# Kernel tuning notes

Measured on AMD Instinct MI355X. Metric: run time of the kernel, lower is better.

## Reference

```python
import jax, jax.numpy as jnp
import numpy as np

EPS = 1e-3  # keras BatchNormalization epsilon=0.001
CLIP = 20.0

def bn(x, g, b, m, v):
    # inference-mode batch norm over last axis
    return (x - m) * jax.lax.rsqrt(v + EPS) * g + b

def conv1d_relu(x, w, b, stride):
    # x: [B,T,C], w: [K,Cin,Cout], VALID padding, relu
    y = jax.lax.conv_general_dilated(x, w, (stride,), 'VALID',
                                     dimension_numbers=('NWC', 'WIO', 'NWC'))
    return jax.nn.relu(y + b)

def gru_dir(xp, Wh, bh, reverse):
    # xp: [B,T,3H] precomputed input projection (x@Wx + input bias)
    # keras GRU, reset_after=True, activation=relu, recurrent_activation=sigmoid
    B, T, H3 = xp.shape
    H = H3 // 3
    def step(h, xt):
        mh = h @ Wh + bh                       # [B,3H]
        xz, xr, xh = jnp.split(xt, 3, axis=-1)
        rz, rr, rh = jnp.split(mh, 3, axis=-1)
        z = jax.nn.sigmoid(xz + rz)
        r = jax.nn.sigmoid(xr + rr)
        hh = jax.nn.relu(xh + r * rh)
        h = z * h + (1.0 - z) * hh
        return h, h
    xs = jnp.swapaxes(xp, 0, 1)                # [T,B,3H]
    h0 = jnp.zeros((B, H), xp.dtype)
    _, ys = jax.lax.scan(step, h0, xs, reverse=reverse)
    return jnp.swapaxes(ys, 0, 1)              # [B,T,H]

def bi_gru_sum(x, Wx, Wh, b):
    # Wx: [2,in,3H], Wh: [2,H,3H], b: [2,2,3H] (input bias, recurrent bias)
    out = None
    for d in range(2):
        xp = x @ Wx[d] + b[d, 0]
        y = gru_dir(xp, Wh[d], b[d, 1], reverse=(d == 1))
        out = y if out is None else out + y
    return out


def setup_inputs() -> dict:
    key = jax.random.key(0)
    ks = jax.random.split(key, 16)
    B, T, F = 16, 1600, 80
    C = 512      # conv filters / gru units / fc units
    K = 5        # kernel size
    L = 3        # bi_gru layers
    V = 6000     # output_dim
    def rn(k, shape, s):
        return (jax.random.normal(k, shape, jnp.float32) * s)
    inp = {
        'x': rn(ks[0], (B, T, F), 1.0),
        'bn1_g': jnp.ones((F,), jnp.float32), 'bn1_b': jnp.zeros((F,), jnp.float32),
        'bn1_m': rn(ks[1], (F,), 0.1), 'bn1_v': jnp.ones((F,), jnp.float32),
        'conv_w0': rn(ks[2], (K, F, C), 0.05), 'conv_b0': jnp.zeros((C,), jnp.float32),
        'conv_w1': rn(ks[3], (K, C, C), 0.02), 'conv_b1': jnp.zeros((C,), jnp.float32),
        'bn2_g': jnp.ones((C,), jnp.float32), 'bn2_b': jnp.zeros((C,), jnp.float32),
        'bn2_m': rn(ks[4], (C,), 0.1), 'bn2_v': jnp.ones((C,), jnp.float32),
        # stacked GRU params: [layers, 2 dirs, ...]; relu recurrence -> small init
        'gru_wx': rn(ks[5], (L, 2, C, 3 * C), 0.03),
        'gru_wh': rn(ks[6], (L, 2, C, 3 * C), 0.03),
        'gru_b': jnp.zeros((L, 2, 2, 3 * C), jnp.float32),
        'bn3_g': jnp.ones((C,), jnp.float32), 'bn3_b': jnp.zeros((C,), jnp.float32),
        'bn3_m': rn(ks[7], (C,), 0.1), 'bn3_v': jnp.ones((C,), jnp.float32),
        'fc_w': rn(ks[8], (C, C), 0.04), 'fc_b': jnp.zeros((C,), jnp.float32),
        'sm_w': rn(ks[9], (C, V), 0.04), 'sm_b': jnp.zeros((V,), jnp.float32),
    }
    return inp


def reference(x, bn1_g, bn1_b, bn1_m, bn1_v,
              conv_w0, conv_b0, conv_w1, conv_b1,
              bn2_g, bn2_b, bn2_m, bn2_v,
              gru_wx, gru_wh, gru_b,
              bn3_g, bn3_b, bn3_m, bn3_v,
              fc_w, fc_b, sm_w, sm_b):
    x = bn(x, bn1_g, bn1_b, bn1_m, bn1_v)
    x = conv1d_relu(x, conv_w0, conv_b0, 2)    # [B,798,512]
    x = conv1d_relu(x, conv_w1, conv_b1, 2)    # [B,397,512]
    x = bn(x, bn2_g, bn2_b, bn2_m, bn2_v)
    for l in range(gru_wx.shape[0]):
        x = bi_gru_sum(x, gru_wx[l], gru_wh[l], gru_b[l])
    x = bn(x, bn3_g, bn3_b, bn3_m, bn3_v)
    x = jnp.minimum(jax.nn.relu(x @ fc_w + fc_b), CLIP)  # clipped_relu(max=20)
    return jax.nn.softmax(x @ sm_w + sm_b, axis=-1)      # [B,397,6000]
```

## Files before the change

kernel.cpp:

```cpp
#include <hip/hip_runtime.h>
#include <math.h>

using bf16x8 = __attribute__((ext_vector_type(8))) short;
using f32x4  = __attribute__((ext_vector_type(4))) float;
typedef unsigned short u16;
typedef unsigned int   u32;

#define EPSBN 1e-3f

__device__ __forceinline__ u16 f2bf(float f){
  union { float f; u32 u; } c; c.f = f;
  u32 u = c.u + 0x7fffu + ((c.u >> 16) & 1u);
  return (u16)(u >> 16);
}
__device__ __forceinline__ float bf2f(u16 b){
  union { u32 u; float f; } c; c.u = ((u32)b) << 16; return c.f;
}
__device__ __forceinline__ void splitstore(float v, u16* ph, u16* pl){
  u16 h = f2bf(v); *ph = h; *pl = f2bf(v - bf2f(h));
}
__device__ __forceinline__ f32x4 MFMA(bf16x8 a, bf16x8 b, f32x4 c){
  return __builtin_amdgcn_mfma_f32_16x16x32_bf16(a, b, c, 0, 0, 0);
}

__device__ __forceinline__ bf16x8 ld128_sys(const u16* p){
  bf16x8 r;
  asm volatile("global_load_dwordx4 %0, %1, off sc0 sc1" : "=v"(r) : "v"(p) : "memory");
  return r;
}
__device__ __forceinline__ void st16_sys(u16* p, u16 v){
  u32 vv = v;
  asm volatile("global_store_short %0, %1, off sc0 sc1" :: "v"(p), "v"(vv) : "memory");
}

__global__ __launch_bounds__(256) void k_bn1_split(
    const float* __restrict__ x, const float* __restrict__ g, const float* __restrict__ b,
    const float* __restrict__ m, const float* __restrict__ v,
    u16* __restrict__ oh, u16* __restrict__ ol)
{
  int i = blockIdx.x*256 + threadIdx.x;
  if (i >= 2048000) return;
  int ci = i % 80;
  float s = g[ci] * rsqrtf(v[ci] + EPSBN);
  float val = (x[i] - m[ci]) * s + b[ci];
  splitstore(val, oh+i, ol+i);
}

__global__ __launch_bounds__(256) void k_prep_c1w(
    const float* __restrict__ w0, u16* __restrict__ oh, u16* __restrict__ ol)
{
  int i = blockIdx.x*256 + threadIdx.x;
  if (i >= 512*416) return;
  int co = i / 416, kf = i - co*416;
  float val = 0.f;
  if (kf < 400){ int kw = kf/80, ci = kf - kw*80; val = w0[(kw*80+ci)*512 + co]; }
  splitstore(val, oh+i, ol+i);
}

__global__ __launch_bounds__(256) void k_prep_c2w(
    const float* __restrict__ w1, u16* __restrict__ oh, u16* __restrict__ ol)
{
  int i = blockIdx.x*256 + threadIdx.x;
  if (i >= 5*512*512) return;
  int co = i & 511, ci = (i >> 9) & 511, kw = i >> 18;
  long o = (long)co*2560 + kw*512 + ci;
  splitstore(w1[i], oh+o, ol+o);
}

__global__ __launch_bounds__(256) void k_prep_wx(
    const float* __restrict__ wx, const float* __restrict__ g2, const float* __restrict__ v2,
    u16* __restrict__ oh, u16* __restrict__ ol)
{
  long i = (long)blockIdx.x*256 + threadIdx.x;
  if (i >= 6L*512*1536) return;
  int n = (int)(i % 1536); long r2 = i / 1536; int k = (int)(r2 % 512); int ld = (int)(r2 / 512);
  float s = (ld < 2) ? g2[k]*rsqrtf(v2[k]+EPSBN) : 1.f;
  long o = ((long)ld*1536 + n)*512 + k;
  splitstore(wx[i]*s, oh+o, ol+o);
}

__global__ __launch_bounds__(256) void k_prep_wh(
    const float* __restrict__ wh, u16* __restrict__ oh, u16* __restrict__ ol)
{
  long i = (long)blockIdx.x*256 + threadIdx.x;
  if (i >= 6L*512*1536) return;
  int n = (int)(i % 1536); long r2 = i / 1536; int k = (int)(r2 % 512); int ld = (int)(r2 / 512);
  long o = ((long)ld*1536 + n)*512 + k;
  splitstore(wh[i], oh+o, ol+o);
}

__global__ __launch_bounds__(256) void k_prep_grub(
    const float* __restrict__ gb, const float* __restrict__ wx,
    const float* __restrict__ g2, const float* __restrict__ b2,
    const float* __restrict__ m2, const float* __restrict__ v2,
    float* __restrict__ xbias, float* __restrict__ hbias)
{
  int i = blockIdx.x*256 + threadIdx.x;
  if (i >= 6*1536) return;
  int n = i % 1536, ld = i / 1536;
  float xv = gb[(ld*2 + 0)*1536 + n];
  float hv = gb[(ld*2 + 1)*1536 + n];
  if (ld < 2){
    float acc = 0.f;
    for (int k = 0; k < 512; ++k){
      float s = g2[k]*rsqrtf(v2[k]+EPSBN);
      float t = b2[k] - m2[k]*s;
      acc += t * wx[((long)ld*512 + k)*1536 + n];
    }
    xv += acc;
  }
  xbias[i] = xv; hbias[i] = hv;
}

__global__ __launch_bounds__(256) void k_prep_fcw(
    const float* __restrict__ fw, const float* __restrict__ g3, const float* __restrict__ v3,
    u16* __restrict__ oh, u16* __restrict__ ol)
{
  int i = blockIdx.x*256 + threadIdx.x;
  if (i >= 512*512) return;
  int n = i & 511, k = i >> 9;
  float s = g3[k]*rsqrtf(v3[k]+EPSBN);
  long o = (long)n*512 + k;
  splitstore(fw[i]*s, oh+o, ol+o);
}

__global__ __launch_bounds__(256) void k_prep_fcb(
    const float* __restrict__ fw, const float* __restrict__ fb,
    const float* __restrict__ g3, const float* __restrict__ b3,
    const float* __restrict__ m3, const float* __restrict__ v3,
    float* __restrict__ ob)
{
  int n = blockIdx.x*256 + threadIdx.x;
  if (n >= 512) return;
  float acc = fb[n];
  for (int k = 0; k < 512; ++k){
    float s = g3[k]*rsqrtf(v3[k]+EPSBN);
    float t = b3[k] - m3[k]*s;
    acc += t * fw[k*512 + n];
  }
  ob[n] = acc;
}

__global__ __launch_bounds__(256) void k_prep_smw(
    const float* __restrict__ sw, u16* __restrict__ oh, u16* __restrict__ ol)
{
  long i = (long)blockIdx.x*256 + threadIdx.x;
  if (i >= 512L*6000) return;
  int n = (int)(i % 6000); int k = (int)(i / 6000);
  long o = (long)n*512 + k;
  splitstore(sw[i], oh+o, ol+o);
}

__global__ __launch_bounds__(256) void k_sumsplit(
    const float* __restrict__ a, const float* __restrict__ b,
    u16* __restrict__ oh, u16* __restrict__ ol)
{
  int i = blockIdx.x*256 + threadIdx.x;
  if (i >= 6352*512) return;
  splitstore(a[i] + b[i], oh+i, ol+i);
}

template<int AMODE, int EPI>
__global__ __launch_bounds__(256,1)
void gemm_split(const u16* __restrict__ Ah, const u16* __restrict__ Al,
                const u16* __restrict__ Bh, const u16* __restrict__ Bl,
                const float* __restrict__ bias,
                float* __restrict__ outF, u16* __restrict__ outH, u16* __restrict__ outL,
                int M, int N, int K, int Kvalid, int TIN, int TOUT)
{
  constexpr int CW = (AMODE==1) ? 80 : 512;
  const int tid  = threadIdx.x;
  const int lane = tid & 63;
  const int w    = tid >> 6;
  const int wm = w >> 1, wn = w & 1;
  const int r  = lane & 15, kg = lane >> 4;
  const int m0 = blockIdx.y * 64 + wm * 32;
  const int n0 = blockIdx.x * 64 + wn * 32;

  long abase[2];
  #pragma unroll
  for (int mt = 0; mt < 2; ++mt){
    int m = m0 + mt*16 + r;
    int mc = m < M ? m : M - 1;
    if (AMODE == 0) abase[mt] = (long)mc * K;
    else { int bb = mc / TOUT; int tt = mc - bb * TOUT; abase[mt] = ((long)bb * TIN + 2*tt) * CW; }
  }
  long bbase[2];
  #pragma unroll
  for (int nt = 0; nt < 2; ++nt){
    int n = n0 + nt*16 + r;
    int nc = n < N ? n : N - 1;
    bbase[nt] = (long)nc * K;
  }

  f32x4 acc[2][2];
  #pragma unroll
  for (int a_ = 0; a_ < 2; ++a_)
    #pragma unroll
    for (int b_ = 0; b_ < 2; ++b_) acc[a_][b_] = f32x4{0.f,0.f,0.f,0.f};

  const bf16x8 zfrag = {0,0,0,0,0,0,0,0};
  const int koff = kg * 8;
  const int KT = K >> 5;
  for (int kt = 0; kt < KT; ++kt){
    int kf = kt*32 + koff;
    bf16x8 ah[2], al[2], bh[2], bl[2];
    #pragma unroll
    for (int nt = 0; nt < 2; ++nt){
      bh[nt] = *(const bf16x8*)(Bh + bbase[nt] + kf);
      bl[nt] = *(const bf16x8*)(Bl + bbase[nt] + kf);
    }
    #pragma unroll
    for (int mt = 0; mt < 2; ++mt){
      if (AMODE == 0){
        long ao = abase[mt] + kf;
        ah[mt] = *(const bf16x8*)(Ah + ao); al[mt] = *(const bf16x8*)(Al + ao);
      } else {
        if (kf < Kvalid){
          int kw = kf / CW; int ci = kf - kw*CW;
          long ao = abase[mt] + (long)kw*CW + ci;
          ah[mt] = *(const bf16x8*)(Ah + ao); al[mt] = *(const bf16x8*)(Al + ao);
        } else { ah[mt] = zfrag; al[mt] = zfrag; }
      }
    }
    #pragma unroll
    for (int mt = 0; mt < 2; ++mt)
      #pragma unroll
      for (int nt = 0; nt < 2; ++nt){
        acc[mt][nt] = MFMA(ah[mt], bh[nt], acc[mt][nt]);
        acc[mt][nt] = MFMA(ah[mt], bl[nt], acc[mt][nt]);
        acc[mt][nt] = MFMA(al[mt], bh[nt], acc[mt][nt]);
      }
  }

  #pragma unroll
  for (int nt = 0; nt < 2; ++nt){
    int n = n0 + nt*16 + r;
    if (n >= N) continue;
    float bv = bias ? bias[n] : 0.f;
    #pragma unroll
    for (int mt = 0; mt < 2; ++mt){
      #pragma unroll
      for (int q = 0; q < 4; ++q){
        int m = m0 + mt*16 + kg*4 + q;
        if (m >= M) continue;
        float v = acc[mt][nt][q] + bv;
        if (EPI == 1) v = fmaxf(v, 0.f);
        if (EPI == 2) v = fminf(fmaxf(v, 0.f), 20.f);
        long o = (long)m * N + n;
        if (EPI == 0) outF[o] = v;
        else { u16 h = f2bf(v); outH[o] = h; outL[o] = f2bf(v - bf2f(h)); }
      }
    }
  }
}

__global__ __launch_bounds__(256,1)
void gru_layer(const float* __restrict__ xp,
               const u16* __restrict__ WhH, const u16* __restrict__ WhL,
               const float* __restrict__ hbias,
               float* __restrict__ yf, float* __restrict__ yb,
               u16* __restrict__ hbH_, u16* __restrict__ hbL_,
               u32* __restrict__ flags)
{
  const int dir = blockIdx.x >> 5;
  const int s   = blockIdx.x & 31;
  const int tid = threadIdx.x, lane = tid & 63, w = tid >> 6;
  const int r = lane & 15, kg = lane >> 4;

  const float* xpd = xp + (long)dir * (6352L*1536);
  const u16* whh = WhH + (long)dir * (1536L*512);
  const u16* whl = WhL + (long)dir * (1536L*512);
  const float* hb = hbias + dir * 1536;
  float* y = dir ? yb : yf;
  u16* hbH = hbH_ + dir * (2*8192);
  u16* hbL = hbL_ + dir * (2*8192);
  u32* flg = flags + dir * 32;

  __shared__ float red[4][3][64][4];

  bf16x8 Bh[3][4], Bl[3][4];
  #pragma unroll
  for (int g = 0; g < 3; ++g){
    long nb = (long)(g*512 + s*16 + r) * 512;
    #pragma unroll
    for (int kk = 0; kk < 4; ++kk){
      int k = (w*4 + kk)*32 + kg*8;
      Bh[g][kk] = *(const bf16x8*)(whh + nb + k);
      Bl[g][kk] = *(const bf16x8*)(whl + nb + k);
    }
  }

  const int gb = tid >> 4, gj = tid & 15;
  const int gcol = s*16 + gj;
  const float bz = hb[gcol], br = hb[512 + gcol], bhh = hb[1024 + gcol];
  const int rl = ((gb >> 2) << 4) | gj;
  const int rq = gb & 3;
  const int rb = r * 512 + kg * 8;
  float hreg = 0.f;

  for (int t = 0; t < 397; ++t){
    #pragma unroll
    for (int g = 0; g < 3; ++g)
      #pragma unroll
      for (int kk = 0; kk < 4; ++kk)
        asm volatile("" : "+v"(Bh[g][kk]), "+v"(Bl[g][kk]));

    const int tpos = dir ? (396 - t) : t;
    const long xb_ = ((long)gb*397 + tpos)*1536 + gcol;
    float xz = xpd[xb_], xr = xpd[xb_ + 512], xh = xpd[xb_ + 1024];

    f32x4 a0 = f32x4{0.f,0.f,0.f,0.f}, a1 = a0, a2 = a0;
    if (t > 0){
      if (w == 0){
        const u32 tgt = (u32)t;
        for (;;){
          int done = 1;
          if (lane < 32)
            done = (__hip_atomic_load(flg + lane, __ATOMIC_RELAXED,
                                      __HIP_MEMORY_SCOPE_AGENT) >= tgt);
          if (__all(done)) break;
        }
      }
      __syncthreads();
      const u16* hH = hbH + (t & 1) * 8192;
      const u16* hL = hbL + (t & 1) * 8192;
      bf16x8 ah[4], al[4];
      #pragma unroll
      for (int kk = 0; kk < 4; ++kk){
        int k = (w*4 + kk) * 32;
        ah[kk] = ld128_sys(hH + rb + k);
        al[kk] = ld128_sys(hL + rb + k);
      }
      asm volatile("s_waitcnt vmcnt(0)" ::: "memory");
      __builtin_amdgcn_sched_barrier(0);
      #pragma unroll
      for (int kk = 0; kk < 4; ++kk){
        a0 = MFMA(ah[kk], Bh[0][kk], a0); a0 = MFMA(ah[kk], Bl[0][kk], a0); a0 = MFMA(al[kk], Bh[0][kk], a0);
        a1 = MFMA(ah[kk], Bh[1][kk], a1); a1 = MFMA(ah[kk], Bl[1][kk], a1); a1 = MFMA(al[kk], Bh[1][kk], a1);
        a2 = MFMA(ah[kk], Bh[2][kk], a2); a2 = MFMA(ah[kk], Bl[2][kk], a2); a2 = MFMA(al[kk], Bh[2][kk], a2);
      }
    }
    *(f32x4*)&red[w][0][lane][0] = a0;
    *(f32x4*)&red[w][1][lane][0] = a1;
    *(f32x4*)&red[w][2][lane][0] = a2;
    __syncthreads();
    float rz = bz, rr = br, rh = bhh;
    #pragma unroll
    for (int ww = 0; ww < 4; ++ww){
      rz += red[ww][0][rl][rq];
      rr += red[ww][1][rl][rq];
      rh += red[ww][2][rl][rq];
    }
    float z  = 1.f / (1.f + __expf(-(xz + rz)));
    float rg = 1.f / (1.f + __expf(-(xr + rr)));
    float hh = fmaxf(xh + rg * rh, 0.f);
    hreg = z * hreg + (1.f - z) * hh;

    {
      u16* oH = hbH + ((t+1) & 1) * 8192;
      u16* oL = hbL + ((t+1) & 1) * 8192;
      u16 hhi = f2bf(hreg);
      u16 hlo = f2bf(hreg - bf2f(hhi));
      st16_sys(oH + gb*512 + gcol, hhi);
      st16_sys(oL + gb*512 + gcol, hlo);
    }
    asm volatile("s_waitcnt vmcnt(0)" ::: "memory");
    __syncthreads();
    if (tid == 0)
      __hip_atomic_store(flg + s, (u32)(t + 1), __ATOMIC_RELAXED,
                         __HIP_MEMORY_SCOPE_AGENT);
    y[((long)gb*397 + tpos)*512 + gcol] = hreg;
  }
}

__global__ __launch_bounds__(256,1) void k_softmax(float* __restrict__ out)
{
  const int tid = threadIdx.x;
  float* prow = out + (long)blockIdx.x * 6000;
  float vals[24];
  float mx = -3.0e38f;
  #pragma unroll
  for (int i = 0; i < 24; ++i){
    int idx = tid + i*256;
    vals[i] = (idx < 6000) ? prow[idx] : -3.0e38f;
    mx = fmaxf(mx, vals[i]);
  }
  #pragma unroll
  for (int o = 32; o; o >>= 1) mx = fmaxf(mx, __shfl_xor(mx, o));
  __shared__ float sred[4];
  if ((tid & 63) == 0) sred[tid >> 6] = mx;
  __syncthreads();
  mx = fmaxf(fmaxf(sred[0], sred[1]), fmaxf(sred[2], sred[3]));
  __syncthreads();
  float sum = 0.f;
  #pragma unroll
  for (int i = 0; i < 24; ++i){
    int idx = tid + i*256;
    vals[i] = (idx < 6000) ? expf(vals[i] - mx) : 0.f;
    sum += vals[i];
  }
  #pragma unroll
  for (int o = 32; o; o >>= 1) sum += __shfl_xor(sum, o);
  if ((tid & 63) == 0) sred[tid >> 6] = sum;
  __syncthreads();
  sum = sred[0] + sred[1] + sred[2] + sred[3];
  float inv = 1.f / sum;
  #pragma unroll
  for (int i = 0; i < 24; ++i){
    int idx = tid + i*256;
    if (idx < 6000) prow[idx] = vals[i] * inv;
  }
}

extern "C" void kernel_launch(void* const* d_in, const int* in_sizes, int n_in,
                              void* d_out, int out_size, void* d_ws, size_t ws_size,
                              hipStream_t stream)
{
  (void)in_sizes; (void)n_in; (void)out_size; (void)ws_size;
  const float* x    = (const float*)d_in[0];
  const float* bn1g = (const float*)d_in[1];
  const float* bn1b = (const float*)d_in[2];
  const float* bn1m = (const float*)d_in[3];
  const float* bn1v = (const float*)d_in[4];
  const float* cw0  = (const float*)d_in[5];
  const float* cb0  = (const float*)d_in[6];
  const float* cw1  = (const float*)d_in[7];
  const float* cb1  = (const float*)d_in[8];
  const float* bn2g = (const float*)d_in[9];
  const float* bn2b = (const float*)d_in[10];
  const float* bn2m = (const float*)d_in[11];
  const float* bn2v = (const float*)d_in[12];
  const float* gwx  = (const float*)d_in[13];
  const float* gwh  = (const float*)d_in[14];
  const float* gbia = (const float*)d_in[15];
  const float* bn3g = (const float*)d_in[16];
  const float* bn3b = (const float*)d_in[17];
  const float* bn3m = (const float*)d_in[18];
  const float* bn3v = (const float*)d_in[19];
  const float* fcw  = (const float*)d_in[20];
  const float* fcb  = (const float*)d_in[21];
  const float* smw  = (const float*)d_in[22];
  const float* smb  = (const float*)d_in[23];

  char* p = (char*)d_ws;
  auto alloc = [&](size_t bytes)->char*{
    char* q = p; p += (bytes + 255) & ~(size_t)255; return q;
  };
  const size_t NX=2048000, NC1W=512*416, NC1O=12768L*512, NC2W=512*2560,
               NC2O=6352L*512, NWX=6L*1536*512, NXP=2L*6352*1536,
               NSMW=6000L*512, NFCW=512*512, NHB=2L*2*8192;

  u16 *xbnH=(u16*)alloc(NX*2),  *xbnL=(u16*)alloc(NX*2);
  u16 *c1wH=(u16*)alloc(NC1W*2),*c1wL=(u16*)alloc(NC1W*2);
  u16 *c1oH=(u16*)alloc(NC1O*2),*c1oL=(u16*)alloc(NC1O*2);
  u16 *c2wH=(u16*)alloc(NC2W*2),*c2wL=(u16*)alloc(NC2W*2);
  u16 *c2oH=(u16*)alloc(NC2O*2),*c2oL=(u16*)alloc(NC2O*2);
  u16 *wxH=(u16*)alloc(NWX*2),  *wxL=(u16*)alloc(NWX*2);
  u16 *whH=(u16*)alloc(NWX*2),  *whL=(u16*)alloc(NWX*2);
  float *xbias=(float*)alloc(6*1536*4), *hbias=(float*)alloc(6*1536*4);
  float *xp=(float*)alloc(NXP*4);
  float *yf=(float*)alloc(NC2O*4), *yb=(float*)alloc(NC2O*4);
  u16 *ysH=(u16*)alloc(NC2O*2), *ysL=(u16*)alloc(NC2O*2);
  u16 *fcwH=(u16*)alloc(NFCW*2),*fcwL=(u16*)alloc(NFCW*2);
  float *fcb2=(float*)alloc(512*4);
  u16 *fcoH=(u16*)alloc(NC2O*2),*fcoL=(u16*)alloc(NC2O*2);
  u16 *smwH=(u16*)alloc(NSMW*2),*smwL=(u16*)alloc(NSMW*2);
  u16 *hbH=(u16*)alloc(NHB*2),  *hbL=(u16*)alloc(NHB*2);
  u32 *flags=(u32*)alloc(3*64*4);

  hipMemsetAsync(flags, 0, 3*64*4, stream);

  k_bn1_split<<<8000,256,0,stream>>>(x, bn1g,bn1b,bn1m,bn1v, xbnH,xbnL);
  k_prep_c1w <<<832,256,0,stream>>>(cw0, c1wH,c1wL);
  k_prep_c2w <<<5120,256,0,stream>>>(cw1, c2wH,c2wL);
  k_prep_wx  <<<18432,256,0,stream>>>(gwx, bn2g,bn2v, wxH,wxL);
  k_prep_wh  <<<18432,256,0,stream>>>(gwh, whH,whL);
  k_prep_grub<<<36,256,0,stream>>>(gbia, gwx, bn2g,bn2b,bn2m,bn2v, xbias,hbias);
  k_prep_fcw <<<1024,256,0,stream>>>(fcw, bn3g,bn3v, fcwH,fcwL);
  k_prep_fcb <<<2,256,0,stream>>>(fcw,fcb, bn3g,bn3b,bn3m,bn3v, fcb2);
  k_prep_smw <<<12000,256,0,stream>>>(smw, smwH,smwL);

  gemm_split<1,1><<<dim3(8,200),256,0,stream>>>(xbnH,xbnL, c1wH,c1wL, cb0,
      nullptr, c1oH,c1oL, 12768,512,416, 400, 1600,798);
  gemm_split<2,1><<<dim3(8,100),256,0,stream>>>(c1oH,c1oL, c2wH,c2wL, cb1,
      nullptr, c2oH,c2oL, 6352,512,2560, 2560, 798,397);

  const u16 *aH = c2oH, *aL = c2oL;
  for (int l = 0; l < 3; ++l){
    for (int d = 0; d < 2; ++d){
      gemm_split<0,0><<<dim3(24,100),256,0,stream>>>(aH,aL,
          wxH + (size_t)(l*2+d)*786432, wxL + (size_t)(l*2+d)*786432,
          xbias + (l*2+d)*1536,
          xp + (size_t)d*9756672, nullptr,nullptr,
          6352,1536,512, 512, 0,0);
    }
    gru_layer<<<64,256,0,stream>>>(xp,
        whH + (size_t)l*2*786432, whL + (size_t)l*2*786432,
        hbias + l*2*1536, yf,yb, hbH,hbL, flags + l*64);
    k_sumsplit<<<12704,256,0,stream>>>(yf,yb, ysH,ysL);
    aH = ysH; aL = ysL;
  }

  gemm_split<0,2><<<dim3(8,100),256,0,stream>>>(ysH,ysL, fcwH,fcwL, fcb2,
      nullptr, fcoH,fcoL, 6352,512,512, 512, 0,0);
  gemm_split<0,0><<<dim3(94,100),256,0,stream>>>(fcoH,fcoL, smwH,smwL, smb,
      (float*)d_out, nullptr,nullptr, 6352,6000,512, 512, 0,0);
  k_softmax<<<6352,256,0,stream>>>((float*)d_out);
}
```

Baseline: 5.924 ms.

## Halve GRU persistent blocks so each block owns 32 hidden columns

The persistent GRU recurrence kernel now runs 16 blocks per direction instead of 32, and each block computes 32 hidden columns (6 MFMA column tiles) rather than 16. This halves the number of flags each block polls at every timestep, shrinking the cross-block barrier cost that dominates the sequential scan. Flag loads and stores switch to inline system-coherent dword asm instead of HIP atomics. In exchange each block holds twice the recurrent weights in registers and does twice the MFMA work per step, which raises register pressure and may lengthen the per-step critical path.

```diff
diff --git a/kernel.cpp b/kernel.cpp
--- a/kernel.cpp
+++ b/kernel.cpp
@@ -31,6 +31,15 @@
 __device__ __forceinline__ void st16_sys(u16* p, u16 v){
   u32 vv = v;
   asm volatile("global_store_short %0, %1, off sc0 sc1" :: "v"(p), "v"(vv) : "memory");
+}
+__device__ __forceinline__ u32 ld32_sys(const u32* p){
+  u32 r;
+  asm volatile("global_load_dword %0, %1, off sc0 sc1\n\ts_waitcnt vmcnt(0)"
+               : "=v"(r) : "v"(p) : "memory");
+  return r;
+}
+__device__ __forceinline__ void st32_sys(u32* p, u32 v){
+  asm volatile("global_store_dword %0, %1, off sc0 sc1" :: "v"(p), "v"(v) : "memory");
 }
 
 __global__ __launch_bounds__(256) void k_bn1_split(
@@ -263,8 +272,8 @@
                u16* __restrict__ hbH_, u16* __restrict__ hbL_,
                u32* __restrict__ flags)
 {
-  const int dir = blockIdx.x >> 5;
-  const int s   = blockIdx.x & 31;
+  const int dir = blockIdx.x >> 4;
+  const int s   = blockIdx.x & 15;
   const int tid = threadIdx.x, lane = tid & 63, w = tid >> 6;
   const int r = lane & 15, kg = lane >> 4;
 
@@ -275,50 +284,48 @@
   float* y = dir ? yb : yf;
   u16* hbH = hbH_ + dir * (2*8192);
   u16* hbL = hbL_ + dir * (2*8192);
-  u32* flg = flags + dir * 32;
-
-  __shared__ float red[4][3][64][4];
-
-  bf16x8 Bh[3][4], Bl[3][4];
-  #pragma unroll
-  for (int g = 0; g < 3; ++g){
-    long nb = (long)(g*512 + s*16 + r) * 512;
+  u32* flg = flags + dir * 16;
+
+  __shared__ float red[4][6][64][4];
+
+  bf16x8 Bh[6][4], Bl[6][4];
+  #pragma unroll
+  for (int ct = 0; ct < 6; ++ct){
+    int g = ct >> 1, chh = ct & 1;
+    long nb = (long)(g*512 + s*32 + chh*16 + r) * 512;
     #pragma unroll
     for (int kk = 0; kk < 4; ++kk){
       int k = (w*4 + kk)*32 + kg*8;
-      Bh[g][kk] = *(const bf16x8*)(whh + nb + k);
-      Bl[g][kk] = *(const bf16x8*)(whl + nb + k);
-    }
-  }
-
-  const int gb = tid >> 4, gj = tid & 15;
-  const int gcol = s*16 + gj;
-  const float bz = hb[gcol], br = hb[512 + gcol], bhh = hb[1024 + gcol];
-  const int rl = ((gb >> 2) << 4) | gj;
+      Bh[ct][kk] = *(const bf16x8*)(whh + nb + k);
+      Bl[ct][kk] = *(const bf16x8*)(whl + nb + k);
+    }
+  }
+
+  const int gb = tid >> 4, cj = tid & 15;
+  const int gc0 = s*32 + cj, gc1 = gc0 + 16;
+  const float bz0=hb[gc0], br0=hb[512+gc0], bh0=hb[1024+gc0];
+  const float bz1=hb[gc1], br1=hb[512+gc1], bh1=hb[1024+gc1];
+  const int rl = ((gb >> 2) << 4) | cj;
   const int rq = gb & 3;
   const int rb = r * 512 + kg * 8;
-  float hreg = 0.f;
+  float h0 = 0.f, h1 = 0.f;
 
   for (int t = 0; t < 397; ++t){
-    #pragma unroll
-    for (int g = 0; g < 3; ++g)
-      #pragma unroll
-      for (int kk = 0; kk < 4; ++kk)
-        asm volatile("" : "+v"(Bh[g][kk]), "+v"(Bl[g][kk]));
-
     const int tpos = dir ? (396 - t) : t;
-    const long xb_ = ((long)gb*397 + tpos)*1536 + gcol;
-    float xz = xpd[xb_], xr = xpd[xb_ + 512], xh = xpd[xb_ + 1024];
-
-    f32x4 a0 = f32x4{0.f,0.f,0.f,0.f}, a1 = a0, a2 = a0;
+    const long xb_ = ((long)gb*397 + tpos)*1536;
+    float xz0 = xpd[xb_+gc0], xr0 = xpd[xb_+512+gc0], xh0 = xpd[xb_+1024+gc0];
+    float xz1 = xpd[xb_+gc1], xr1 = xpd[xb_+512+gc1], xh1 = xpd[xb_+1024+gc1];
+
+    f32x4 acc[6];
+    #pragma unroll
+    for (int ct = 0; ct < 6; ++ct) acc[ct] = f32x4{0.f,0.f,0.f,0.f};
+
     if (t > 0){
       if (w == 0){
         const u32 tgt = (u32)t;
         for (;;){
           int done = 1;
-          if (lane < 32)
-            done = (__hip_atomic_load(flg + lane, __ATOMIC_RELAXED,
-                                      __HIP_MEMORY_SCOPE_AGENT) >= tgt);
+          if (lane < 16) done = (ld32_sys(flg + lane) >= tgt);
           if (__all(done)) break;
         }
       }
@@ -335,42 +342,50 @@
       asm volatile("s_waitcnt vmcnt(0)" ::: "memory");
       __builtin_amdgcn_sched_barrier(0);
       #pragma unroll
-      for (int kk = 0; kk < 4; ++kk){
-        a0 = MFMA(ah[kk], Bh[0][kk], a0); a0 = MFMA(ah[kk], Bl[0][kk], a0); a0 = MFMA(al[kk], Bh[0][kk], a0);
-        a1 = MFMA(ah[kk], Bh[1][kk], a1); a1 = MFMA(ah[kk], Bl[1][kk], a1); a1 = MFMA(al[kk], Bh[1][kk], a1);
-        a2 = MFMA(ah[kk], Bh[2][kk], a2); a2 = MFMA(ah[kk], Bl[2][kk], a2); a2 = MFMA(al[kk], Bh[2][kk], a2);
-      }
-    }
-    *(f32x4*)&red[w][0][lane][0] = a0;
-    *(f32x4*)&red[w][1][lane][0] = a1;
-    *(f32x4*)&red[w][2][lane][0] = a2;
+      for (int kk = 0; kk < 4; ++kk)
+        #pragma unroll
+        for (int ct = 0; ct < 6; ++ct){
+          acc[ct] = MFMA(ah[kk], Bh[ct][kk], acc[ct]);
+          acc[ct] = MFMA(ah[kk], Bl[ct][kk], acc[ct]);
+          acc[ct] = MFMA(al[kk], Bh[ct][kk], acc[ct]);
+        }
+    }
+    #pragma unroll
+    for (int ct = 0; ct < 6; ++ct)
+      *(f32x4*)&red[w][ct][lane][0] = acc[ct];
     __syncthreads();
-    float rz = bz, rr = br, rh = bhh;
+
+    float rz0=bz0, rr0=br0, rh0=bh0, rz1=bz1, rr1=br1, rh1=bh1;
     #pragma unroll
     for (int ww = 0; ww < 4; ++ww){
-      rz += red[ww][0][rl][rq];
-      rr += red[ww][1][rl][rq];
-      rh += red[ww][2][rl][rq];
-    }
-    float z  = 1.f / (1.f + __expf(-(xz + rz)));
-    float rg = 1.f / (1.f + __expf(-(xr + rr)));
-    float hh = fmaxf(xh + rg * rh, 0.f);
-    hreg = z * hreg + (1.f - z) * hh;
+      rz0 += red[ww][0][rl][rq]; rz1 += red[ww][1][rl][rq];
+      rr0 += red[ww][2][rl][rq]; rr1 += red[ww][3][rl][rq];
+      rh0 += red[ww][4][rl][rq]; rh1 += red[ww][5][rl][rq];
+    }
+    float z0  = 1.f / (1.f + __expf(-(xz0 + rz0)));
+    float g0  = 1.f / (1.f + __expf(-(xr0 + rr0)));
+    float hh0 = fmaxf(xh0 + g0 * rh0, 0.f);
+    h0 = z0 * h0 + (1.f - z0) * hh0;
+    float z1  = 1.f / (1.f + __expf(-(xz1 + rz1)));
+    float g1  = 1.f / (1.f + __expf(-(xr1 + rr1)));
+    float hh1 = fmaxf(xh1 + g1 * rh1, 0.f);
+    h1 = z1 * h1 + (1.f - z1) * hh1;
 
     {
       u16* oH = hbH + ((t+1) & 1) * 8192;
       u16* oL = hbL + ((t+1) & 1) * 8192;
-      u16 hhi = f2bf(hreg);
-      u16 hlo = f2bf(hreg - bf2f(hhi));
-      st16_sys(oH + gb*512 + gcol, hhi);
-      st16_sys(oL + gb*512 + gcol, hlo);
+      u16 a = f2bf(h0); u16 b = f2bf(h0 - bf2f(a));
+      u16 c = f2bf(h1); u16 d = f2bf(h1 - bf2f(c));
+      st16_sys(oH + gb*512 + gc0, a);
+      st16_sys(oL + gb*512 + gc0, b);
+      st16_sys(oH + gb*512 + gc1, c);
+      st16_sys(oL + gb*512 + gc1, d);
     }
     asm volatile("s_waitcnt vmcnt(0)" ::: "memory");
     __syncthreads();
-    if (tid == 0)
-      __hip_atomic_store(flg + s, (u32)(t + 1), __ATOMIC_RELAXED,
-                         __HIP_MEMORY_SCOPE_AGENT);
-    y[((long)gb*397 + tpos)*512 + gcol] = hreg;
+    if (tid == 0) st32_sys(flg + s, (u32)(t + 1));
+    y[((long)gb*397 + tpos)*512 + gc0] = h0;
+    y[((long)gb*397 + tpos)*512 + gc1] = h1;
   }
 }
 
@@ -467,9 +482,9 @@
   u16 *fcoH=(u16*)alloc(NC2O*2),*fcoL=(u16*)alloc(NC2O*2);
   u16 *smwH=(u16*)alloc(NSMW*2),*smwL=(u16*)alloc(NSMW*2);
   u16 *hbH=(u16*)alloc(NHB*2),  *hbL=(u16*)alloc(NHB*2);
-  u32 *flags=(u32*)alloc(3*64*4);
-
-  hipMemsetAsync(flags, 0, 3*64*4, stream);
+  u32 *flags=(u32*)alloc(4096);
+
+  hipMemsetAsync(flags, 0, 4096, stream);
 
   k_bn1_split<<<8000,256,0,stream>>>(x, bn1g,bn1b,bn1m,bn1v, xbnH,xbnL);
   k_prep_c1w <<<832,256,0,stream>>>(cw0, c1wH,c1wL);
@@ -495,9 +510,9 @@
           xp + (size_t)d*9756672, nullptr,nullptr,
           6352,1536,512, 512, 0,0);
     }
-    gru_layer<<<64,256,0,stream>>>(xp,
+    gru_layer<<<32,256,0,stream>>>(xp,
         whH + (size_t)l*2*786432, whL + (size_t)l*2*786432,
-        hbias + l*2*1536, yf,yb, hbH,hbL, flags + l*64);
+        hbias + l*2*1536, yf,yb, hbH,hbL, flags + l*32);
     k_sumsplit<<<12704,256,0,stream>>>(yf,yb, ysH,ysL);
     aH = ysH; aL = ysL;
   }
```

Result: slower. 6.626 ms (+11.8%).

## Replace GRU flag handshake with timestep-tagged hidden-state words polled directly

Applied to the files above, without the earlier changes.

The cross-block GRU recurrence no longer publishes a per-block flag after a wait-for-stores and a barrier. Each hidden value is now stored as its hi/lo bf16 pair packed together with the timestep tag in one 64-bit system-scope store. Consumers spin on loading the data itself until every tag matches, then unpack the pairs with byte-permute. This removes the separate flag round trip, one block barrier per step and the store-drain wait, and the shared reduction buffer is double-buffered so it stays safe without that barrier. In exchange each step reads twice as many bytes. The buffer is never initialised, so correctness relies on leftover tags from a previous layer or call not matching the expected timestep.

```diff
diff --git a/kernel.cpp b/kernel.cpp
--- a/kernel.cpp
+++ b/kernel.cpp
@@ -3,6 +3,8 @@
 
 using bf16x8 = __attribute__((ext_vector_type(8))) short;
 using f32x4  = __attribute__((ext_vector_type(4))) float;
+using u32x2  = __attribute__((ext_vector_type(2))) unsigned int;
+using u32x4  = __attribute__((ext_vector_type(4))) unsigned int;
 typedef unsigned short u16;
 typedef unsigned int   u32;
 
@@ -23,14 +25,14 @@
   return __builtin_amdgcn_mfma_f32_16x16x32_bf16(a, b, c, 0, 0, 0);
 }
 
-__device__ __forceinline__ bf16x8 ld128_sys(const u16* p){
-  bf16x8 r;
+__device__ __forceinline__ u32x4 ldq_sys(const u32* p){
+  u32x4 r;
   asm volatile("global_load_dwordx4 %0, %1, off sc0 sc1" : "=v"(r) : "v"(p) : "memory");
   return r;
 }
-__device__ __forceinline__ void st16_sys(u16* p, u16 v){
-  u32 vv = v;
-  asm volatile("global_store_short %0, %1, off sc0 sc1" :: "v"(p), "v"(vv) : "memory");
+__device__ __forceinline__ void st64_sys(u32* p, u32 w0, u32 w1){
+  u32x2 v; v.x = w0; v.y = w1;
+  asm volatile("global_store_dwordx2 %0, %1, off sc0 sc1" :: "v"(p), "v"(v) : "memory");
 }
 
 __global__ __launch_bounds__(256) void k_bn1_split(
@@ -260,8 +262,7 @@
                const u16* __restrict__ WhH, const u16* __restrict__ WhL,
                const float* __restrict__ hbias,
                float* __restrict__ yf, float* __restrict__ yb,
-               u16* __restrict__ hbH_, u16* __restrict__ hbL_,
-               u32* __restrict__ flags)
+               u32* __restrict__ hq_)
 {
   const int dir = blockIdx.x >> 5;
   const int s   = blockIdx.x & 31;
@@ -273,11 +274,9 @@
   const u16* whl = WhL + (long)dir * (1536L*512);
   const float* hb = hbias + dir * 1536;
   float* y = dir ? yb : yf;
-  u16* hbH = hbH_ + dir * (2*8192);
-  u16* hbL = hbL_ + dir * (2*8192);
-  u32* flg = flags + dir * 32;
-
-  __shared__ float red[4][3][64][4];
+  u32* hq = hq_ + dir * 32768;
+
+  __shared__ float red[2][4][3][64][4];
 
   bf16x8 Bh[3][4], Bl[3][4];
   #pragma unroll
@@ -296,44 +295,52 @@
   const float bz = hb[gcol], br = hb[512 + gcol], bhh = hb[1024 + gcol];
   const int rl = ((gb >> 2) << 4) | gj;
   const int rq = gb & 3;
-  const int rb = r * 512 + kg * 8;
+  const int cb0 = r * 512 + kg * 8;
   float hreg = 0.f;
 
   for (int t = 0; t < 397; ++t){
-    #pragma unroll
-    for (int g = 0; g < 3; ++g)
-      #pragma unroll
-      for (int kk = 0; kk < 4; ++kk)
-        asm volatile("" : "+v"(Bh[g][kk]), "+v"(Bl[g][kk]));
-
     const int tpos = dir ? (396 - t) : t;
     const long xb_ = ((long)gb*397 + tpos)*1536 + gcol;
     float xz = xpd[xb_], xr = xpd[xb_ + 512], xh = xpd[xb_ + 1024];
 
     f32x4 a0 = f32x4{0.f,0.f,0.f,0.f}, a1 = a0, a2 = a0;
     if (t > 0){
-      if (w == 0){
-        const u32 tgt = (u32)t;
-        for (;;){
-          int done = 1;
-          if (lane < 32)
-            done = (__hip_atomic_load(flg + lane, __ATOMIC_RELAXED,
-                                      __HIP_MEMORY_SCOPE_AGENT) >= tgt);
-          if (__all(done)) break;
-        }
+      const u32 tt = (u32)t;
+      const u32* hqb = hq + (t & 1) * 16384;
+      const u32* pk[4];
+      #pragma unroll
+      for (int kk = 0; kk < 4; ++kk)
+        pk[kk] = hqb + ((cb0 + (w*4 + kk)*32) << 1);
+
+      u32x4 q[4][4];
+      for (;;){
+        #pragma unroll
+        for (int kk = 0; kk < 4; ++kk)
+          #pragma unroll
+          for (int j = 0; j < 4; ++j)
+            q[kk][j] = ldq_sys(pk[kk] + j*4);
+        asm volatile("s_waitcnt vmcnt(0)" ::: "memory");
+        u32 bad = 0;
+        #pragma unroll
+        for (int kk = 0; kk < 4; ++kk)
+          #pragma unroll
+          for (int j = 0; j < 4; ++j)
+            bad |= (q[kk][j].y ^ tt) | (q[kk][j].w ^ tt);
+        if (__all(bad == 0)) break;
       }
-      __syncthreads();
-      const u16* hH = hbH + (t & 1) * 8192;
-      const u16* hL = hbL + (t & 1) * 8192;
+      __builtin_amdgcn_sched_barrier(0);
+
       bf16x8 ah[4], al[4];
       #pragma unroll
       for (int kk = 0; kk < 4; ++kk){
-        int k = (w*4 + kk) * 32;
-        ah[kk] = ld128_sys(hH + rb + k);
-        al[kk] = ld128_sys(hL + rb + k);
+        union { bf16x8 v; u32 u[4]; } A, L;
+        #pragma unroll
+        for (int j = 0; j < 4; ++j){
+          A.u[j] = __builtin_amdgcn_perm(q[kk][j].z, q[kk][j].x, 0x07060302u);
+          L.u[j] = __builtin_amdgcn_perm(q[kk][j].z, q[kk][j].x, 0x05040100u);
+        }
+        ah[kk] = A.v; al[kk] = L.v;
       }
-      asm volatile("s_waitcnt vmcnt(0)" ::: "memory");
-      __builtin_amdgcn_sched_barrier(0);
       #pragma unroll
       for (int kk = 0; kk < 4; ++kk){
         a0 = MFMA(ah[kk], Bh[0][kk], a0); a0 = MFMA(ah[kk], Bl[0][kk], a0); a0 = MFMA(al[kk], Bh[0][kk], a0);
@@ -341,16 +348,17 @@
         a2 = MFMA(ah[kk], Bh[2][kk], a2); a2 = MFMA(ah[kk], Bl[2][kk], a2); a2 = MFMA(al[kk], Bh[2][kk], a2);
       }
     }
-    *(f32x4*)&red[w][0][lane][0] = a0;
-    *(f32x4*)&red[w][1][lane][0] = a1;
-    *(f32x4*)&red[w][2][lane][0] = a2;
+    const int tb = t & 1;
+    *(f32x4*)&red[tb][w][0][lane][0] = a0;
+    *(f32x4*)&red[tb][w][1][lane][0] = a1;
+    *(f32x4*)&red[tb][w][2][lane][0] = a2;
     __syncthreads();
     float rz = bz, rr = br, rh = bhh;
     #pragma unroll
     for (int ww = 0; ww < 4; ++ww){
-      rz += red[ww][0][rl][rq];
-      rr += red[ww][1][rl][rq];
-      rh += red[ww][2][rl][rq];
+      rz += red[tb][ww][0][rl][rq];
+      rr += red[tb][ww][1][rl][rq];
+      rh += red[tb][ww][2][rl][rq];
     }
     float z  = 1.f / (1.f + __expf(-(xz + rz)));
     float rg = 1.f / (1.f + __expf(-(xr + rr)));
@@ -358,18 +366,10 @@
     hreg = z * hreg + (1.f - z) * hh;
 
     {
-      u16* oH = hbH + ((t+1) & 1) * 8192;
-      u16* oL = hbL + ((t+1) & 1) * 8192;
-      u16 hhi = f2bf(hreg);
-      u16 hlo = f2bf(hreg - bf2f(hhi));
-      st16_sys(oH + gb*512 + gcol, hhi);
-      st16_sys(oL + gb*512 + gcol, hlo);
-    }
-    asm volatile("s_waitcnt vmcnt(0)" ::: "memory");
-    __syncthreads();
-    if (tid == 0)
-      __hip_atomic_store(flg + s, (u32)(t + 1), __ATOMIC_RELAXED,
-                         __HIP_MEMORY_SCOPE_AGENT);
+      u32* o = hq + ((t+1) & 1) * 16384 + ((gb*512 + gcol) << 1);
+      u16 hi = f2bf(hreg); u16 lo = f2bf(hreg - bf2f(hi));
+      st64_sys(o, ((u32)hi << 16) | (u32)lo, (u32)(t + 1));
+    }
     y[((long)gb*397 + tpos)*512 + gcol] = hreg;
   }
 }
@@ -449,7 +449,7 @@
   };
   const size_t NX=2048000, NC1W=512*416, NC1O=12768L*512, NC2W=512*2560,
                NC2O=6352L*512, NWX=6L*1536*512, NXP=2L*6352*1536,
-               NSMW=6000L*512, NFCW=512*512, NHB=2L*2*8192;
+               NSMW=6000L*512, NFCW=512*512;
 
   u16 *xbnH=(u16*)alloc(NX*2),  *xbnL=(u16*)alloc(NX*2);
   u16 *c1wH=(u16*)alloc(NC1W*2),*c1wL=(u16*)alloc(NC1W*2);
@@ -466,10 +466,7 @@
   float *fcb2=(float*)alloc(512*4);
   u16 *fcoH=(u16*)alloc(NC2O*2),*fcoL=(u16*)alloc(NC2O*2);
   u16 *smwH=(u16*)alloc(NSMW*2),*smwL=(u16*)alloc(NSMW*2);
-  u16 *hbH=(u16*)alloc(NHB*2),  *hbL=(u16*)alloc(NHB*2);
-  u32 *flags=(u32*)alloc(3*64*4);
-
-  hipMemsetAsync(flags, 0, 3*64*4, stream);
+  u32 *hq=(u32*)alloc(2L*2*16*512*2*4);
 
   k_bn1_split<<<8000,256,0,stream>>>(x, bn1g,bn1b,bn1m,bn1v, xbnH,xbnL);
   k_prep_c1w <<<832,256,0,stream>>>(cw0, c1wH,c1wL);
@@ -497,7 +494,7 @@
     }
     gru_layer<<<64,256,0,stream>>>(xp,
         whH + (size_t)l*2*786432, whL + (size_t)l*2*786432,
-        hbias + l*2*1536, yf,yb, hbH,hbL, flags + l*64);
+        hbias + l*2*1536, yf,yb, hq);
     k_sumsplit<<<12704,256,0,stream>>>(yf,yb, ysH,ysL);
     aH = ysH; aL = ysL;
   }
```

Result: slower. 7.058 ms (+19.1%).
